# Kernel tuning notes

Measured on AMD Instinct MI355X. Metric: run time of the kernel, lower is better.

## Reference

```python
import jax, jax.numpy as jnp
import numpy as np

B, S, H, L = 64, 512, 768, 21


def setup_inputs() -> dict:
    key = jax.random.key(0)
    ks = jax.random.split(key, 8)
    hidden = jax.random.normal(ks[0], (B, S, H), dtype=jnp.float32)
    attention_mask = jnp.ones((B, S), dtype=jnp.int32)
    labels = jax.random.randint(ks[1], (B, S), 0, L, dtype=jnp.int64)
    W = jax.random.normal(ks[2], (H, L), dtype=jnp.float32) * 0.02
    b = jnp.zeros((L,), dtype=jnp.float32)
    start_transitions = jax.random.uniform(ks[3], (L,), minval=-0.1, maxval=0.1)
    end_transitions = jax.random.uniform(ks[4], (L,), minval=-0.1, maxval=0.1)
    transitions = jax.random.uniform(ks[5], (L, L), minval=-0.1, maxval=0.1)
    return {"hidden": hidden, "attention_mask": attention_mask, "labels": labels,
            "W": W, "b": b, "start_transitions": start_transitions,
            "end_transitions": end_transitions, "transitions": transitions}


def _crf_llh(emissions, tags, mask, start, end, trans):
    # torchcrf log-likelihood, batch_first. emissions [B,S,L], tags [B,S], mask [B,S] bool
    maskf = mask.astype(emissions.dtype)
    first_tags = tags[:, 0]
    num = start[first_tags] + jnp.take_along_axis(emissions[:, 0], first_tags[:, None], axis=1)[:, 0]
    trans_scores = trans[tags[:, :-1], tags[:, 1:]]                         # [B,S-1]
    emit_scores = jnp.take_along_axis(emissions, tags[:, :, None], axis=2)[:, :, 0]  # [B,S]
    num = num + jnp.sum((trans_scores + emit_scores[:, 1:]) * maskf[:, 1:], axis=1)
    seq_ends = jnp.sum(mask.astype(jnp.int32), axis=1) - 1
    last_tags = jnp.take_along_axis(tags, seq_ends[:, None], axis=1)[:, 0]
    num = num + end[last_tags]
    # denominator: forward algorithm as a scan over time
    def step(score, xs):
        emit_t, m_t = xs  # [B,L], [B]
        nxt = jax.nn.logsumexp(score[:, :, None] + trans[None] + emit_t[:, None, :], axis=1)
        return jnp.where(m_t[:, None], nxt, score), None
    score0 = start[None] + emissions[:, 0]
    xs = (jnp.transpose(emissions[:, 1:], (1, 0, 2)), mask[:, 1:].T)
    scoreT, _ = jax.lax.scan(step, score0, xs)
    denom = jax.nn.logsumexp(scoreT + end[None], axis=1)
    return num - denom


def _viterbi_one_hot(emissions, mask, start, end, trans):
    # Viterbi decode (max-plus scan) + backtrack, returns one-hot logits like _decoded_to_one_hot
    def fstep(score, xs):
        emit_t, m_t = xs
        cand = score[:, :, None] + trans[None]     # [B,L,L]
        idx = jnp.argmax(cand, axis=1)             # [B,L] best previous tag
        nxt = jnp.max(cand, axis=1) + emit_t
        return jnp.where(m_t[:, None], nxt, score), idx
    score0 = start[None] + emissions[:, 0]
    xs = (jnp.transpose(emissions[:, 1:], (1, 0, 2)), mask[:, 1:].T)
    scoreT, hist = jax.lax.scan(fstep, score0, xs)   # hist [S-1,B,L]
    best_last = jnp.argmax(scoreT + end[None], axis=1)  # [B]
    def bstep(carry, xs):
        h_t, m_t = xs
        prev = jnp.take_along_axis(h_t, carry[:, None], axis=1)[:, 0]
        return jnp.where(m_t, prev, carry), carry
    tag0, tags_rest = jax.lax.scan(bstep, best_last, (hist, mask[:, 1:].T), reverse=True)
    tags = jnp.concatenate([tag0[:, None], tags_rest.T], axis=1)  # [B,S]
    one_hot = jax.nn.one_hot(tags, emissions.shape[-1], dtype=emissions.dtype)
    return one_hot * mask[:, :, None].astype(emissions.dtype)


def reference(hidden, attention_mask, labels, W, b, start_transitions, end_transitions, transitions):
    mask = attention_mask.astype(bool)
    emissions = jnp.einsum('bsh,hl->bsl', hidden, W) + b  # classifier (dropout = identity in eval)
    logits = _viterbi_one_hot(emissions, mask, start_transitions, end_transitions, transitions)
    # loss path: replicate forward's tag/mask fixups
    tags = jnp.where(labels < 0, 0, labels).at[:, 0].set(0)
    valid = (mask & (labels >= 0)).at[:, 0].set(True)
    llh = _crf_llh(emissions, tags, valid, start_transitions, end_transitions, transitions)
    loss = -jnp.mean(llh)
    return loss, logits
```

## Files before the change

kernel.cpp:

```cpp
#include <hip/hip_runtime.h>
#include <math.h>

#define BB 64
#define SS 512
#define HH 768
#define LL 21
#define STR 513
#define INFF __builtin_huge_valf()

__device__ inline float rlf(float v, int i) {
    return __int_as_float(__builtin_amdgcn_readlane(__float_as_int(v), i));
}
__device__ inline float mx3(float a, float b, float c) { return fmaxf(fmaxf(a, b), c); }
__device__ inline float wmax64(float v) {
    #pragma unroll
    for (int off = 32; off; off >>= 1) v = fmaxf(v, __shfl_xor(v, off));
    return v;
}
__device__ inline float rlmax21(float a) {
    float r0 = mx3(rlf(a, 0), rlf(a, 1), rlf(a, 2));
    float r1 = mx3(rlf(a, 3), rlf(a, 4), rlf(a, 5));
    float r2 = mx3(rlf(a, 6), rlf(a, 7), rlf(a, 8));
    float r3 = mx3(rlf(a, 9), rlf(a, 10), rlf(a, 11));
    float r4 = mx3(rlf(a, 12), rlf(a, 13), rlf(a, 14));
    float r5 = mx3(rlf(a, 15), rlf(a, 16), rlf(a, 17));
    float r6 = mx3(rlf(a, 18), rlf(a, 19), rlf(a, 20));
    return mx3(mx3(r0, r1, r2), mx3(r3, r4, r5), r6);
}

__global__ __launch_bounds__(128) void k_emis(const float* __restrict__ hidden,
                                              const float* __restrict__ W,
                                              const float* __restrict__ bias,
                                              float* __restrict__ em0,
                                              float* __restrict__ em1) {
    __shared__ float Wl[384 * 24];
    int tid = threadIdx.x;
    int half = blockIdx.x & 1;
    int rb = blockIdx.x >> 1;
    int row = rb * 128 + tid;
    const float* hp = hidden + (size_t)row * HH + half * 384;
    const float4* Wh4 = reinterpret_cast<const float4*>(W + half * 384 * LL);

    for (int f = tid; f < 2016; f += 128) {
        float4 v = Wh4[f];
        int e0 = 4 * f;
        { int e = e0,     k = e / 21, l = e - 21 * k; Wl[k * 24 + l] = v.x; }
        { int e = e0 + 1, k = e / 21, l = e - 21 * k; Wl[k * 24 + l] = v.y; }
        { int e = e0 + 2, k = e / 21, l = e - 21 * k; Wl[k * 24 + l] = v.z; }
        { int e = e0 + 3, k = e / 21, l = e - 21 * k; Wl[k * 24 + l] = v.w; }
    }
    __syncthreads();

    float acc[LL];
    #pragma unroll
    for (int l = 0; l < LL; ++l) acc[l] = 0.f;

#define FMAK(HV, WB) do { \
    float hv_ = (HV); \
    float4 q0 = *reinterpret_cast<const float4*>(WB); \
    float4 q1 = *reinterpret_cast<const float4*>((WB) + 4); \
    float4 q2 = *reinterpret_cast<const float4*>((WB) + 8); \
    float4 q3 = *reinterpret_cast<const float4*>((WB) + 12); \
    float4 q4 = *reinterpret_cast<const float4*>((WB) + 16); \
    float q20 = (WB)[20]; \
    acc[0]  = fmaf(hv_, q0.x, acc[0]);  acc[1]  = fmaf(hv_, q0.y, acc[1]); \
    acc[2]  = fmaf(hv_, q0.z, acc[2]);  acc[3]  = fmaf(hv_, q0.w, acc[3]); \
    acc[4]  = fmaf(hv_, q1.x, acc[4]);  acc[5]  = fmaf(hv_, q1.y, acc[5]); \
    acc[6]  = fmaf(hv_, q1.z, acc[6]);  acc[7]  = fmaf(hv_, q1.w, acc[7]); \
    acc[8]  = fmaf(hv_, q2.x, acc[8]);  acc[9]  = fmaf(hv_, q2.y, acc[9]); \
    acc[10] = fmaf(hv_, q2.z, acc[10]); acc[11] = fmaf(hv_, q2.w, acc[11]); \
    acc[12] = fmaf(hv_, q3.x, acc[12]); acc[13] = fmaf(hv_, q3.y, acc[13]); \
    acc[14] = fmaf(hv_, q3.z, acc[14]); acc[15] = fmaf(hv_, q3.w, acc[15]); \
    acc[16] = fmaf(hv_, q4.x, acc[16]); acc[17] = fmaf(hv_, q4.y, acc[17]); \
    acc[18] = fmaf(hv_, q4.z, acc[18]); acc[19] = fmaf(hv_, q4.w, acc[19]); \
    acc[20] = fmaf(hv_, q20, acc[20]); } while (0)

    float4 ha = *reinterpret_cast<const float4*>(hp);
    for (int c = 0; c < 96; ++c) {
        float4 hn = ha;
        if (c + 1 < 96) hn = *reinterpret_cast<const float4*>(hp + (c + 1) * 4);
        const float* wb = Wl + (c * 4) * 24;
        FMAK(ha.x, wb);
        FMAK(ha.y, wb + 24);
        FMAK(ha.z, wb + 48);
        FMAK(ha.w, wb + 72);
        ha = hn;
    }
#undef FMAK

    float* emr = (half ? em1 : em0) + (size_t)row * LL;
    if (half) {
        #pragma unroll
        for (int l = 0; l < LL; ++l) emr[l] = acc[l];
    } else {
        #pragma unroll
        for (int l = 0; l < LL; ++l) emr[l] = acc[l] + bias[l];
    }
}

__global__ __launch_bounds__(64) void k_scan(const float* __restrict__ em0,
                                             const float* __restrict__ em1,
                                             const int* __restrict__ attn,
                                             const int* __restrict__ labels,
                                             const float* __restrict__ startT,
                                             const float* __restrict__ endT,
                                             const float* __restrict__ trans,
                                             float* __restrict__ num,
                                             float* __restrict__ denom,
                                             float* __restrict__ Sout) {
    __shared__ float eLT[LL * STR + 8];
    int lane = threadIdx.x;
    int bid = blockIdx.x;
    bool act = lane < LL;
    int jj = act ? lane : (LL - 1);

    if (bid < 128) {
        int b = bid & 63;
        const float* emb0 = em0 + (size_t)b * SS * LL;
        const float* emb1 = em1 + (size_t)b * SS * LL;
        const int* mrow = attn + b * SS;

        for (int f = lane; f < (SS * LL) / 4; f += 64) {
            float4 v0 = *reinterpret_cast<const float4*>(emb0 + 4 * f);
            float4 v1 = *reinterpret_cast<const float4*>(emb1 + 4 * f);
            float4 v = make_float4(v0.x + v1.x, v0.y + v1.y, v0.z + v1.z, v0.w + v1.w);
            unsigned e0 = 4u * (unsigned)f;
            { unsigned t = e0 / 21u,       j = e0 - 21u * t;       eLT[j * STR + t] = v.x; }
            { unsigned e = e0 + 1, t = e / 21u, j = e - 21u * t;   eLT[j * STR + t] = v.y; }
            { unsigned e = e0 + 2, t = e / 21u, j = e - 21u * t;   eLT[j * STR + t] = v.z; }
            { unsigned e = e0 + 3, t = e / 21u, j = e - 21u * t;   eLT[j * STR + t] = v.w; }
        }
        __syncthreads();

        int jbase = jj * STR;
        float A0, A1, A2, A3, B0, B1, B2, B3;

#define LDG(P, G) do { int t4_ = (G) * 4; \
    P##0 = eLT[jbase + t4_];     P##1 = eLT[jbase + t4_ + 1]; \
    P##2 = eLT[jbase + t4_ + 2]; P##3 = eLT[jbase + t4_ + 3]; } while (0)

        if (bid < 64) {
            float Tc[LL];
            #pragma unroll
            for (int i = 0; i < LL; ++i) Tc[i] = trans[i * LL + jj];
            float* Sgj = Sout + (size_t)b * (LL * SS) + jj * SS;

#define VCORE(EMIT, BIT) do { \
    float sv_[LL]; \
    _Pragma("unroll") for (int i_ = 0; i_ < LL; ++i_) sv_[i_] = rlf(a, i_); \
    __builtin_amdgcn_sched_barrier(0); \
    float cd_[LL]; \
    _Pragma("unroll") for (int i_ = 0; i_ < LL; ++i_) cd_[i_] = sv_[i_] + Tc[i_]; \
    float x0 = mx3(cd_[0], cd_[1], cd_[2]),   x1 = mx3(cd_[3], cd_[4], cd_[5]); \
    float x2 = mx3(cd_[6], cd_[7], cd_[8]),   x3 = mx3(cd_[9], cd_[10], cd_[11]); \
    float x4 = mx3(cd_[12], cd_[13], cd_[14]), x5 = mx3(cd_[15], cd_[16], cd_[17]); \
    float x6 = mx3(cd_[18], cd_[19], cd_[20]); \
    float best = mx3(mx3(x0, x1, x2), mx3(x3, x4, x5), x6); \
    bool mt_ = ((mm >> (BIT)) & 1ull) != 0ull; \
    float an_ = best + (EMIT); \
    a = (mt_ && act) ? an_ : a; \
} while (0)
#define VGROUPR(P, TB, BB0) do { \
    float o0_, o1_, o2_, o3_; \
    VCORE(P##0, (BB0));     o0_ = a; \
    VCORE(P##1, (BB0) + 1); o1_ = a; \
    VCORE(P##2, (BB0) + 2); o2_ = a; \
    VCORE(P##3, (BB0) + 3); o3_ = a; \
    if (act) *reinterpret_cast<float4*>(Sgj + (TB)) = make_float4(o0_, o1_, o2_, o3_); \
} while (0)

            LDG(A, 0); LDG(B, 1);
            int mk0 = mrow[lane];
            unsigned long long mm = __ballot(mk0 != 0);
            mk0 = mrow[64 + lane];
            float a = act ? (startT[lane] + A0) : -INFF;
            {
                float o0_ = a, o1_, o2_, o3_;
                VCORE(A1, 1); o1_ = a;
                VCORE(A2, 2); o2_ = a;
                VCORE(A3, 3); o3_ = a;
                if (act) *reinterpret_cast<float4*>(Sgj) = make_float4(o0_, o1_, o2_, o3_);
                LDG(A, 2);
                VGROUPR(B, 4, 4);
                LDG(B, 3);
            }
            for (int gg = 1; gg < 64; ++gg) {
                if ((gg & 7) == 0) {
                    mm = __ballot(mk0 != 0);
                    if (gg != 56) mk0 = mrow[((gg >> 3) + 1) * 64 + lane];
                }
                int bb = (gg & 7) * 8;
                VGROUPR(A, 8 * gg, bb);
                LDG(A, 2 * gg + 2);
                VGROUPR(B, 8 * gg + 4, bb + 4);
                LDG(B, 2 * gg + 3);
            }
#undef VCORE
#undef VGROUPR
        } else {
            float Ec[LL];
            #pragma unroll
            for (int i = 0; i < LL; ++i) Ec[i] = __expf(trans[i * LL + jj]);

#define LCORE(EMIT, BIT) do { \
    float x_ = __expf(a - M); \
    float sv_[LL]; \
    _Pragma("unroll") for (int i_ = 0; i_ < LL; ++i_) sv_[i_] = rlf(x_, i_); \
    __builtin_amdgcn_sched_barrier(0); \
    float g0_ = sv_[0] * Ec[0]; \
    _Pragma("unroll") for (int i_ = 1; i_ < 7; ++i_)  g0_ = fmaf(sv_[i_], Ec[i_], g0_); \
    float g1_ = sv_[7] * Ec[7]; \
    _Pragma("unroll") for (int i_ = 8; i_ < 14; ++i_) g1_ = fmaf(sv_[i_], Ec[i_], g1_); \
    float g2_ = sv_[14] * Ec[14]; \
    _Pragma("unroll") for (int i_ = 15; i_ < 21; ++i_) g2_ = fmaf(sv_[i_], Ec[i_], g2_); \
    float Ss_ = (g0_ + g1_) + g2_; \
    bool mt_ = ((mm >> (BIT)) & 1ull) != 0ull; \
    float an_ = M + __logf(Ss_) + (EMIT); \
    a = (mt_ && act) ? an_ : a; \
} while (0)

            LDG(A, 0); LDG(B, 1);
            int mk0 = mrow[lane];
            unsigned long long mm = __ballot(mk0 != 0);
            mk0 = mrow[64 + lane];
            float a = act ? (startT[lane] + A0) : -INFF;
            float M = rlmax21(a);
            {
                LCORE(A1, 1); LCORE(A2, 2); LCORE(A3, 3);
                LDG(A, 2);
                LCORE(B0, 4); LCORE(B1, 5); LCORE(B2, 6); LCORE(B3, 7);
                LDG(B, 3);
            }
            for (int gg = 1; gg < 64; ++gg) {
                if ((gg & 7) == 0) {
                    mm = __ballot(mk0 != 0);
                    if (gg != 56) mk0 = mrow[((gg >> 3) + 1) * 64 + lane];
                }
                M = rlmax21(a);
                int bb = (gg & 7) * 8;
                LCORE(A0, bb);     LCORE(A1, bb + 1); LCORE(A2, bb + 2); LCORE(A3, bb + 3);
                LDG(A, 2 * gg + 2);
                LCORE(B0, bb + 4); LCORE(B1, bb + 5); LCORE(B2, bb + 6); LCORE(B3, bb + 7);
                LDG(B, 2 * gg + 3);
            }
#undef LCORE
            float f = act ? (a + endT[lane]) : -INFF;
            float m = wmax64(f);
            float p = act ? __expf(f - m) : 0.f;
            #pragma unroll
            for (int off = 32; off; off >>= 1) p += __shfl_xor(p, off);
            if (lane == 0) denom[b] = m + __logf(p);
        }
#undef LDG
    } else {
        int b = bid - 128;
        const int* lrow = labels + b * SS;
        const int* arow = attn + b * SS;
        float psum = 0.f;
        int pcnt = 0;
        for (int s = 0; s < 8; ++s) {
            int t = s * 64 + lane;
            int lab = lrow[t];
            int mk = arow[t];
            int valid = (t == 0) ? 1 : ((mk != 0 && lab >= 0) ? 1 : 0);
            if (t >= 1 && valid) {
                int tag = (lab < 0) ? 0 : lab;
                int labp = lrow[t - 1];
                int tagp = (t == 1) ? 0 : ((labp < 0) ? 0 : labp);
                size_t ei = ((size_t)b * SS + t) * LL + tag;
                psum += trans[tagp * LL + tag] + em0[ei] + em1[ei];
            }
            pcnt += valid;
        }
        #pragma unroll
        for (int off = 32; off; off >>= 1) {
            psum += __shfl_xor(psum, off);
            pcnt += __shfl_xor(pcnt, off);
        }
        int ts = pcnt - 1;
        int labL = lrow[ts];
        int tagL = (ts == 0) ? 0 : ((labL < 0) ? 0 : labL);
        if (lane == 0) {
            size_t e0i = (size_t)b * SS * LL;
            num[b] = startT[0] + em0[e0i] + em1[e0i] + psum + endT[tagL];
        }
    }
}

__global__ __launch_bounds__(256) void k_back(const float* __restrict__ S,
                                              const int* __restrict__ attn,
                                              const float* __restrict__ endT,
                                              const float* __restrict__ trans,
                                              int* __restrict__ tagsOut) {
    __shared__ float Sl[LL][517];
    __shared__ unsigned char pred[SS * 24];
    __shared__ unsigned char mapL[64 * 32];
    __shared__ float Tl[441];
    int tid = threadIdx.x, b = blockIdx.x;
    const float* SB = S + (size_t)b * (LL * SS);
    for (int i = tid; i < 441; i += 256) Tl[i] = trans[i];
    for (int f = tid; f < (LL * SS) / 4; f += 256) {
        float4 v = *reinterpret_cast<const float4*>(SB + 4 * f);
        int j = f >> 7, t0 = (f & 127) * 4;
        Sl[j][t0] = v.x; Sl[j][t0 + 1] = v.y; Sl[j][t0 + 2] = v.z; Sl[j][t0 + 3] = v.w;
    }
    __syncthreads();

    for (int u = tid; u < 511 * LL; u += 256) {
        int t = 1 + u / LL;
        int j = u - (u / LL) * LL;
        unsigned int pj = (unsigned int)j;
        if (attn[b * SS + t] != 0) {
            float bv = Sl[0][t - 1] + Tl[j];
            unsigned int bi = 0;
            #pragma unroll
            for (int i = 1; i < LL; ++i) {
                float c = Sl[i][t - 1] + Tl[i * LL + j];
                bool g = c > bv;
                bv = g ? c : bv;
                bi = g ? (unsigned int)i : bi;
            }
            pj = bi;
        }
        pred[t * 24 + j] = (unsigned char)pj;
    }
    __syncthreads();

    if (tid < 64) {
        int lane = tid;
        float f = (lane < LL) ? (Sl[lane][SS - 1] + endT[lane]) : -INFF;
        float m = wmax64(f);
        unsigned long long msk = __ballot(f == m);
        int best_last = __ffsll(msk) - 1;

        int tlo = 8 * lane + 1;
        int thi = 8 * lane + 8; if (thi > 511) thi = 511;
        unsigned int BM[LL];
        #pragma unroll
        for (int s = 0; s < LL; ++s) BM[s] = s;
        for (int k = 0; k < 8; ++k) {
            int t = thi - k;
            if (t >= tlo) {
                #pragma unroll
                for (int s = 0; s < LL; ++s) BM[s] = pred[t * 24 + BM[s]];
            }
        }
        #pragma unroll
        for (int s = 0; s < LL; ++s) mapL[lane * 32 + s] = (unsigned char)BM[s];

        #pragma unroll
        for (int kk = 1; kk < 64; kk <<= 1) {
            int p = lane + kk;
            bool vld = p < 64;
            int pp = vld ? p : 0;
            unsigned int P[LL];
            #pragma unroll
            for (int s = 0; s < LL; ++s) {
                unsigned int v = mapL[pp * 32 + s];
                P[s] = vld ? v : (unsigned int)s;
            }
            unsigned int N[LL];
            #pragma unroll
            for (int s = 0; s < LL; ++s) N[s] = mapL[lane * 32 + P[s]];
            #pragma unroll
            for (int s = 0; s < LL; ++s) mapL[lane * 32 + s] = (unsigned char)N[s];
        }

        int st8 = mapL[lane * 32 + best_last];
        int nxt = __shfl(st8, lane + 1);
        int cur = (lane == 63) ? best_last : nxt;
        for (int k = 0; k < 8; ++k) {
            int t = thi - k;
            if (t >= tlo) {
                tagsOut[b * SS + t] = cur;
                cur = pred[t * 24 + cur];
            }
        }
        if (lane == 0) tagsOut[b * SS] = cur;
    }
}

__global__ __launch_bounds__(256) void k_out(const float* __restrict__ num,
                                             const float* __restrict__ denom,
                                             const int* __restrict__ tagsW,
                                             const int* __restrict__ attn,
                                             float* __restrict__ out) {
    int gid = blockIdx.x * 256 + threadIdx.x;
    if ((int)blockIdx.x == (int)gridDim.x - 1 && threadIdx.x < 64) {
        float llh = num[threadIdx.x] - denom[threadIdx.x];
        #pragma unroll
        for (int off = 32; off; off >>= 1) llh += __shfl_xor(llh, off);
        if (threadIdx.x == 0) out[0] = -llh / (float)BB;
    }
    if (gid < BB * SS * LL) {
        int bt = gid / LL, l = gid % LL;
        int tag = tagsW[bt];
        int mk  = attn[bt];
        out[1 + gid] = (mk && tag == l) ? 1.f : 0.f;
    }
}

extern "C" void kernel_launch(void* const* d_in, const int* in_sizes, int n_in,
                              void* d_out, int out_size, void* d_ws, size_t ws_size,
                              hipStream_t stream) {
    const float* hidden = (const float*)d_in[0];
    const int*   attn   = (const int*)d_in[1];
    const int*   labels = (const int*)d_in[2];
    const float* W      = (const float*)d_in[3];
    const float* bias   = (const float*)d_in[4];
    const float* startT = (const float*)d_in[5];
    const float* endT   = (const float*)d_in[6];
    const float* trans  = (const float*)d_in[7];
    float* out = (float*)d_out;

    float* wsf   = (float*)d_ws;
    float* em0   = wsf;
    float* em1   = em0 + (size_t)BB * SS * LL;
    float* num   = em1 + (size_t)BB * SS * LL;
    float* denom = num + 64;
    int*   tags  = (int*)(denom + 64);
    float* Sbuf  = out + 4;

    hipLaunchKernelGGL(k_emis, dim3(512), dim3(128), 0, stream, hidden, W, bias, em0, em1);
    hipLaunchKernelGGL(k_scan, dim3(192), dim3(64),  0, stream, em0, em1, attn, labels,
                       startT, endT, trans, num, denom, Sbuf);
    hipLaunchKernelGGL(k_back, dim3(64),  dim3(256), 0, stream, Sbuf, attn, endT, trans, tags);
    int oh_blocks = (BB * SS * LL + 255) / 256;
    hipLaunchKernelGGL(k_out,  dim3(oh_blocks + 1), dim3(256), 0, stream,
                       num, denom, tags, attn, out);
}
```

Baseline: 160.6 us.

## Drop LDS staging in CRF scan; stream emissions from global with deeper prefetch

The scan kernel no longer copies and transposes each batch's emissions into shared memory before starting the recurrence. Each wave now reads its per-tag emission values straight from the two global partial buffers, prefetching four groups of timesteps ahead instead of two. Waves are packed 12 per 768-thread block, so 16 blocks launch instead of 192 single-wave blocks. This removes the serial staging phase and barrier at the cost of strided global loads (about 21 floats apart) on the critical path and more live registers.

```diff
diff --git a/kernel.cpp b/kernel.cpp
--- a/kernel.cpp
+++ b/kernel.cpp
@@ -5,7 +5,6 @@
 #define SS 512
 #define HH 768
 #define LL 21
-#define STR 513
 #define INFF __builtin_huge_valf()
 
 __device__ inline float rlf(float v, int i) {
@@ -98,48 +97,39 @@
     }
 }
 
-__global__ __launch_bounds__(64) void k_scan(const float* __restrict__ em0,
-                                             const float* __restrict__ em1,
-                                             const int* __restrict__ attn,
-                                             const int* __restrict__ labels,
-                                             const float* __restrict__ startT,
-                                             const float* __restrict__ endT,
-                                             const float* __restrict__ trans,
-                                             float* __restrict__ num,
-                                             float* __restrict__ denom,
-                                             float* __restrict__ Sout) {
-    __shared__ float eLT[LL * STR + 8];
-    int lane = threadIdx.x;
-    int bid = blockIdx.x;
+__global__ __launch_bounds__(768) void k_scan(const float* __restrict__ em0,
+                                              const float* __restrict__ em1,
+                                              const int* __restrict__ attn,
+                                              const int* __restrict__ labels,
+                                              const float* __restrict__ startT,
+                                              const float* __restrict__ endT,
+                                              const float* __restrict__ trans,
+                                              float* __restrict__ num,
+                                              float* __restrict__ denom,
+                                              float* __restrict__ Sout) {
+    int gw = blockIdx.x * 12 + (threadIdx.x >> 6);
+    int lane = threadIdx.x & 63;
     bool act = lane < LL;
     int jj = act ? lane : (LL - 1);
 
-    if (bid < 128) {
-        int b = bid & 63;
-        const float* emb0 = em0 + (size_t)b * SS * LL;
-        const float* emb1 = em1 + (size_t)b * SS * LL;
+    if (gw < 128) {
+        int b = gw & 63;
+        const float* e0p = em0 + (size_t)b * SS * LL;
+        const float* e1p = em1 + (size_t)b * SS * LL;
         const int* mrow = attn + b * SS;
 
-        for (int f = lane; f < (SS * LL) / 4; f += 64) {
-            float4 v0 = *reinterpret_cast<const float4*>(emb0 + 4 * f);
-            float4 v1 = *reinterpret_cast<const float4*>(emb1 + 4 * f);
-            float4 v = make_float4(v0.x + v1.x, v0.y + v1.y, v0.z + v1.z, v0.w + v1.w);
-            unsigned e0 = 4u * (unsigned)f;
-            { unsigned t = e0 / 21u,       j = e0 - 21u * t;       eLT[j * STR + t] = v.x; }
-            { unsigned e = e0 + 1, t = e / 21u, j = e - 21u * t;   eLT[j * STR + t] = v.y; }
-            { unsigned e = e0 + 2, t = e / 21u, j = e - 21u * t;   eLT[j * STR + t] = v.z; }
-            { unsigned e = e0 + 3, t = e / 21u, j = e - 21u * t;   eLT[j * STR + t] = v.w; }
-        }
-        __syncthreads();
-
-        int jbase = jj * STR;
-        float A0, A1, A2, A3, B0, B1, B2, B3;
-
-#define LDG(P, G) do { int t4_ = (G) * 4; \
-    P##0 = eLT[jbase + t4_];     P##1 = eLT[jbase + t4_ + 1]; \
-    P##2 = eLT[jbase + t4_ + 2]; P##3 = eLT[jbase + t4_ + 3]; } while (0)
-
-        if (bid < 64) {
+        float Ae0, Ae1, Ae2, Ae3, Af0, Af1, Af2, Af3;
+        float Be0, Be1, Be2, Be3, Bf0, Bf1, Bf2, Bf3;
+        float Ce0, Ce1, Ce2, Ce3, Cf0, Cf1, Cf2, Cf3;
+        float De0, De1, De2, De3, Df0, Df1, Df2, Df3;
+
+#define LDG(P, G) do { size_t o_ = (size_t)(G) * 4 * LL + jj; \
+    P##e0 = e0p[o_];          P##f0 = e1p[o_]; \
+    P##e1 = e0p[o_ + LL];     P##f1 = e1p[o_ + LL]; \
+    P##e2 = e0p[o_ + 2 * LL]; P##f2 = e1p[o_ + 2 * LL]; \
+    P##e3 = e0p[o_ + 3 * LL]; P##f3 = e1p[o_ + 3 * LL]; } while (0)
+
+        if (gw < 64) {
             float Tc[LL];
             #pragma unroll
             for (int i = 0; i < LL; ++i) Tc[i] = trans[i * LL + jj];
@@ -160,40 +150,43 @@
     float an_ = best + (EMIT); \
     a = (mt_ && act) ? an_ : a; \
 } while (0)
-#define VGROUPR(P, TB, BB0) do { \
+#define VGROUPR(P, TB, BITB) do { \
     float o0_, o1_, o2_, o3_; \
-    VCORE(P##0, (BB0));     o0_ = a; \
-    VCORE(P##1, (BB0) + 1); o1_ = a; \
-    VCORE(P##2, (BB0) + 2); o2_ = a; \
-    VCORE(P##3, (BB0) + 3); o3_ = a; \
+    VCORE(P##e0 + P##f0, (BITB));     o0_ = a; \
+    VCORE(P##e1 + P##f1, (BITB) + 1); o1_ = a; \
+    VCORE(P##e2 + P##f2, (BITB) + 2); o2_ = a; \
+    VCORE(P##e3 + P##f3, (BITB) + 3); o3_ = a; \
     if (act) *reinterpret_cast<float4*>(Sgj + (TB)) = make_float4(o0_, o1_, o2_, o3_); \
 } while (0)
 
-            LDG(A, 0); LDG(B, 1);
-            int mk0 = mrow[lane];
-            unsigned long long mm = __ballot(mk0 != 0);
-            mk0 = mrow[64 + lane];
-            float a = act ? (startT[lane] + A0) : -INFF;
+            LDG(A, 0); LDG(B, 1); LDG(C, 2); LDG(D, 3);
+            int mkc = mrow[lane];
+            unsigned long long mm = __ballot(mkc != 0);
+            mkc = mrow[64 + lane];
+            float a = act ? (startT[lane] + (Ae0 + Af0)) : -INFF;
             {
                 float o0_ = a, o1_, o2_, o3_;
-                VCORE(A1, 1); o1_ = a;
-                VCORE(A2, 2); o2_ = a;
-                VCORE(A3, 3); o3_ = a;
+                VCORE(Ae1 + Af1, 1); o1_ = a;
+                VCORE(Ae2 + Af2, 2); o2_ = a;
+                VCORE(Ae3 + Af3, 3); o3_ = a;
                 if (act) *reinterpret_cast<float4*>(Sgj) = make_float4(o0_, o1_, o2_, o3_);
-                LDG(A, 2);
-                VGROUPR(B, 4, 4);
-                LDG(B, 3);
-            }
-            for (int gg = 1; gg < 64; ++gg) {
-                if ((gg & 7) == 0) {
-                    mm = __ballot(mk0 != 0);
-                    if (gg != 56) mk0 = mrow[((gg >> 3) + 1) * 64 + lane];
+                LDG(A, 4);
+                VGROUPR(B, 4, 4);   LDG(B, 5);
+                VGROUPR(C, 8, 8);   LDG(C, 6);
+                VGROUPR(D, 12, 12); LDG(D, 7);
+            }
+            for (int s = 1; s < 32; ++s) {
+                if ((s & 3) == 0) {
+                    mm = __ballot(mkc != 0);
+                    int blk = s >> 2;
+                    if (blk < 7) mkc = mrow[(blk + 1) * 64 + lane];
                 }
-                int bb = (gg & 7) * 8;
-                VGROUPR(A, 8 * gg, bb);
-                LDG(A, 2 * gg + 2);
-                VGROUPR(B, 8 * gg + 4, bb + 4);
-                LDG(B, 2 * gg + 3);
+                int g0 = 4 * s;
+                int bitb = (g0 & 15) * 4;
+                VGROUPR(A, g0 * 4,      bitb);      if (s < 31) LDG(A, g0 + 4);
+                VGROUPR(B, g0 * 4 + 4,  bitb + 4);  if (s < 31) LDG(B, g0 + 5);
+                VGROUPR(C, g0 * 4 + 8,  bitb + 8);  if (s < 31) LDG(C, g0 + 6);
+                VGROUPR(D, g0 * 4 + 12, bitb + 12); if (s < 31) LDG(D, g0 + 7);
             }
 #undef VCORE
 #undef VGROUPR
@@ -219,29 +212,48 @@
     a = (mt_ && act) ? an_ : a; \
 } while (0)
 
-            LDG(A, 0); LDG(B, 1);
-            int mk0 = mrow[lane];
-            unsigned long long mm = __ballot(mk0 != 0);
-            mk0 = mrow[64 + lane];
-            float a = act ? (startT[lane] + A0) : -INFF;
+            LDG(A, 0); LDG(B, 1); LDG(C, 2); LDG(D, 3);
+            int mkc = mrow[lane];
+            unsigned long long mm = __ballot(mkc != 0);
+            mkc = mrow[64 + lane];
+            float a = act ? (startT[lane] + (Ae0 + Af0)) : -INFF;
             float M = rlmax21(a);
             {
-                LCORE(A1, 1); LCORE(A2, 2); LCORE(A3, 3);
-                LDG(A, 2);
-                LCORE(B0, 4); LCORE(B1, 5); LCORE(B2, 6); LCORE(B3, 7);
-                LDG(B, 3);
-            }
-            for (int gg = 1; gg < 64; ++gg) {
-                if ((gg & 7) == 0) {
-                    mm = __ballot(mk0 != 0);
-                    if (gg != 56) mk0 = mrow[((gg >> 3) + 1) * 64 + lane];
+                LCORE(Ae1 + Af1, 1); LCORE(Ae2 + Af2, 2); LCORE(Ae3 + Af3, 3);
+                LDG(A, 4);
+                LCORE(Be0 + Bf0, 4); LCORE(Be1 + Bf1, 5);
+                LCORE(Be2 + Bf2, 6); LCORE(Be3 + Bf3, 7);
+                LDG(B, 5);
+                M = rlmax21(a);
+                LCORE(Ce0 + Cf0, 8);  LCORE(Ce1 + Cf1, 9);
+                LCORE(Ce2 + Cf2, 10); LCORE(Ce3 + Cf3, 11);
+                LDG(C, 6);
+                LCORE(De0 + Df0, 12); LCORE(De1 + Df1, 13);
+                LCORE(De2 + Df2, 14); LCORE(De3 + Df3, 15);
+                LDG(D, 7);
+            }
+            for (int s = 1; s < 32; ++s) {
+                if ((s & 3) == 0) {
+                    mm = __ballot(mkc != 0);
+                    int blk = s >> 2;
+                    if (blk < 7) mkc = mrow[(blk + 1) * 64 + lane];
                 }
+                int g0 = 4 * s;
+                int bitb = (g0 & 15) * 4;
                 M = rlmax21(a);
-                int bb = (gg & 7) * 8;
-                LCORE(A0, bb);     LCORE(A1, bb + 1); LCORE(A2, bb + 2); LCORE(A3, bb + 3);
-                LDG(A, 2 * gg + 2);
-                LCORE(B0, bb + 4); LCORE(B1, bb + 5); LCORE(B2, bb + 6); LCORE(B3, bb + 7);
-                LDG(B, 2 * gg + 3);
+                LCORE(Ae0 + Af0, bitb);     LCORE(Ae1 + Af1, bitb + 1);
+                LCORE(Ae2 + Af2, bitb + 2); LCORE(Ae3 + Af3, bitb + 3);
+                if (s < 31) LDG(A, g0 + 4);
+                LCORE(Be0 + Bf0, bitb + 4); LCORE(Be1 + Bf1, bitb + 5);
+                LCORE(Be2 + Bf2, bitb + 6); LCORE(Be3 + Bf3, bitb + 7);
+                if (s < 31) LDG(B, g0 + 5);
+                M = rlmax21(a);
+                LCORE(Ce0 + Cf0, bitb + 8);  LCORE(Ce1 + Cf1, bitb + 9);
+                LCORE(Ce2 + Cf2, bitb + 10); LCORE(Ce3 + Cf3, bitb + 11);
+                if (s < 31) LDG(C, g0 + 6);
+                LCORE(De0 + Df0, bitb + 12); LCORE(De1 + Df1, bitb + 13);
+                LCORE(De2 + Df2, bitb + 14); LCORE(De3 + Df3, bitb + 15);
+                if (s < 31) LDG(D, g0 + 7);
             }
 #undef LCORE
             float f = act ? (a + endT[lane]) : -INFF;
@@ -253,7 +265,7 @@
         }
 #undef LDG
     } else {
-        int b = bid - 128;
+        int b = gw - 128;
         const int* lrow = labels + b * SS;
         const int* arow = attn + b * SS;
         float psum = 0.f;
@@ -422,7 +434,7 @@
     float* Sbuf  = out + 4;
 
     hipLaunchKernelGGL(k_emis, dim3(512), dim3(128), 0, stream, hidden, W, bias, em0, em1);
-    hipLaunchKernelGGL(k_scan, dim3(192), dim3(64),  0, stream, em0, em1, attn, labels,
+    hipLaunchKernelGGL(k_scan, dim3(16),  dim3(768), 0, stream, em0, em1, attn, labels,
                        startT, endT, trans, num, denom, Sbuf);
     hipLaunchKernelGGL(k_back, dim3(64),  dim3(256), 0, stream, Sbuf, attn, endT, trans, tags);
     int oh_blocks = (BB * SS * LL + 255) / 256;
```

After: 279.2 us. 1.74x slower.

## Split emission GEMV into four H-quarters and widen backtrack blocks to 512

Applied to the files above, without the earlier changes.

The emission projection now splits the hidden dimension into four quarters instead of two, launching 1024 blocks, each with a smaller shared W tile. This raises the block count so the GPU's compute units are better filled. The scan kernel sums four partial buffers instead of two, which adds global reads and workspace. The backtrack kernel also goes from 256 to 512 threads per block to speed up the predecessor computation, at the cost of more registers per block.

```diff
diff --git a/kernel.cpp b/kernel.cpp
--- a/kernel.cpp
+++ b/kernel.cpp
@@ -32,17 +32,19 @@
                                               const float* __restrict__ W,
                                               const float* __restrict__ bias,
                                               float* __restrict__ em0,
-                                              float* __restrict__ em1) {
-    __shared__ float Wl[384 * 24];
+                                              float* __restrict__ em1,
+                                              float* __restrict__ em2,
+                                              float* __restrict__ em3) {
+    __shared__ float Wl[192 * 24];
     int tid = threadIdx.x;
-    int half = blockIdx.x & 1;
-    int rb = blockIdx.x >> 1;
-    int row = rb * 128 + tid;
-    const float* hp = hidden + (size_t)row * HH + half * 384;
-    const float4* Wh4 = reinterpret_cast<const float4*>(W + half * 384 * LL);
-
-    for (int f = tid; f < 2016; f += 128) {
-        float4 v = Wh4[f];
+    int q = blockIdx.x & 3;
+    int rg = blockIdx.x >> 2;
+    int row = rg * 128 + tid;
+    const float* hp = hidden + (size_t)row * HH + q * 192;
+    const float4* Wq4 = reinterpret_cast<const float4*>(W + q * 192 * LL);
+
+    for (int f = tid; f < 1008; f += 128) {
+        float4 v = Wq4[f];
         int e0 = 4 * f;
         { int e = e0,     k = e / 21, l = e - 21 * k; Wl[k * 24 + l] = v.x; }
         { int e = e0 + 1, k = e / 21, l = e - 21 * k; Wl[k * 24 + l] = v.y; }
@@ -76,9 +78,9 @@
     acc[20] = fmaf(hv_, q20, acc[20]); } while (0)
 
     float4 ha = *reinterpret_cast<const float4*>(hp);
-    for (int c = 0; c < 96; ++c) {
+    for (int c = 0; c < 48; ++c) {
         float4 hn = ha;
-        if (c + 1 < 96) hn = *reinterpret_cast<const float4*>(hp + (c + 1) * 4);
+        if (c + 1 < 48) hn = *reinterpret_cast<const float4*>(hp + (c + 1) * 4);
         const float* wb = Wl + (c * 4) * 24;
         FMAK(ha.x, wb);
         FMAK(ha.y, wb + 24);
@@ -88,18 +90,20 @@
     }
 #undef FMAK
 
-    float* emr = (half ? em1 : em0) + (size_t)row * LL;
-    if (half) {
+    float* emr = (q == 0 ? em0 : q == 1 ? em1 : q == 2 ? em2 : em3) + (size_t)row * LL;
+    if (q == 0) {
+        #pragma unroll
+        for (int l = 0; l < LL; ++l) emr[l] = acc[l] + bias[l];
+    } else {
         #pragma unroll
         for (int l = 0; l < LL; ++l) emr[l] = acc[l];
-    } else {
-        #pragma unroll
-        for (int l = 0; l < LL; ++l) emr[l] = acc[l] + bias[l];
     }
 }
 
 __global__ __launch_bounds__(64) void k_scan(const float* __restrict__ em0,
                                              const float* __restrict__ em1,
+                                             const float* __restrict__ em2,
+                                             const float* __restrict__ em3,
                                              const int* __restrict__ attn,
                                              const int* __restrict__ labels,
                                              const float* __restrict__ startT,
@@ -116,14 +120,22 @@
 
     if (bid < 128) {
         int b = bid & 63;
-        const float* emb0 = em0 + (size_t)b * SS * LL;
-        const float* emb1 = em1 + (size_t)b * SS * LL;
+        size_t boff = (size_t)b * SS * LL;
+        const float* emb0 = em0 + boff;
+        const float* emb1 = em1 + boff;
+        const float* emb2 = em2 + boff;
+        const float* emb3 = em3 + boff;
         const int* mrow = attn + b * SS;
 
         for (int f = lane; f < (SS * LL) / 4; f += 64) {
             float4 v0 = *reinterpret_cast<const float4*>(emb0 + 4 * f);
             float4 v1 = *reinterpret_cast<const float4*>(emb1 + 4 * f);
-            float4 v = make_float4(v0.x + v1.x, v0.y + v1.y, v0.z + v1.z, v0.w + v1.w);
+            float4 v2 = *reinterpret_cast<const float4*>(emb2 + 4 * f);
+            float4 v3 = *reinterpret_cast<const float4*>(emb3 + 4 * f);
+            float4 v = make_float4((v0.x + v1.x) + (v2.x + v3.x),
+                                   (v0.y + v1.y) + (v2.y + v3.y),
+                                   (v0.z + v1.z) + (v2.z + v3.z),
+                                   (v0.w + v1.w) + (v2.w + v3.w));
             unsigned e0 = 4u * (unsigned)f;
             { unsigned t = e0 / 21u,       j = e0 - 21u * t;       eLT[j * STR + t] = v.x; }
             { unsigned e = e0 + 1, t = e / 21u, j = e - 21u * t;   eLT[j * STR + t] = v.y; }
@@ -268,7 +280,7 @@
                 int labp = lrow[t - 1];
                 int tagp = (t == 1) ? 0 : ((labp < 0) ? 0 : labp);
                 size_t ei = ((size_t)b * SS + t) * LL + tag;
-                psum += trans[tagp * LL + tag] + em0[ei] + em1[ei];
+                psum += trans[tagp * LL + tag] + ((em0[ei] + em1[ei]) + (em2[ei] + em3[ei]));
             }
             pcnt += valid;
         }
@@ -282,12 +294,13 @@
         int tagL = (ts == 0) ? 0 : ((labL < 0) ? 0 : labL);
         if (lane == 0) {
             size_t e0i = (size_t)b * SS * LL;
-            num[b] = startT[0] + em0[e0i] + em1[e0i] + psum + endT[tagL];
-        }
-    }
-}
-
-__global__ __launch_bounds__(256) void k_back(const float* __restrict__ S,
+            num[b] = startT[0] + ((em0[e0i] + em1[e0i]) + (em2[e0i] + em3[e0i]))
+                   + psum + endT[tagL];
+        }
+    }
+}
+
+__global__ __launch_bounds__(512) void k_back(const float* __restrict__ S,
                                               const int* __restrict__ attn,
                                               const float* __restrict__ endT,
                                               const float* __restrict__ trans,
@@ -298,15 +311,15 @@
     __shared__ float Tl[441];
     int tid = threadIdx.x, b = blockIdx.x;
     const float* SB = S + (size_t)b * (LL * SS);
-    for (int i = tid; i < 441; i += 256) Tl[i] = trans[i];
-    for (int f = tid; f < (LL * SS) / 4; f += 256) {
+    for (int i = tid; i < 441; i += 512) Tl[i] = trans[i];
+    for (int f = tid; f < (LL * SS) / 4; f += 512) {
         float4 v = *reinterpret_cast<const float4*>(SB + 4 * f);
         int j = f >> 7, t0 = (f & 127) * 4;
         Sl[j][t0] = v.x; Sl[j][t0 + 1] = v.y; Sl[j][t0 + 2] = v.z; Sl[j][t0 + 3] = v.w;
     }
     __syncthreads();
 
-    for (int u = tid; u < 511 * LL; u += 256) {
+    for (int u = tid; u < 511 * LL; u += 512) {
         int t = 1 + u / LL;
         int j = u - (u / LL) * LL;
         unsigned int pj = (unsigned int)j;
@@ -414,17 +427,21 @@
     float* out = (float*)d_out;
 
     float* wsf   = (float*)d_ws;
+    size_t emsz  = (size_t)BB * SS * LL;
     float* em0   = wsf;
-    float* em1   = em0 + (size_t)BB * SS * LL;
-    float* num   = em1 + (size_t)BB * SS * LL;
+    float* em1   = em0 + emsz;
+    float* em2   = em1 + emsz;
+    float* em3   = em2 + emsz;
+    float* num   = em3 + emsz;
     float* denom = num + 64;
     int*   tags  = (int*)(denom + 64);
     float* Sbuf  = out + 4;
 
-    hipLaunchKernelGGL(k_emis, dim3(512), dim3(128), 0, stream, hidden, W, bias, em0, em1);
-    hipLaunchKernelGGL(k_scan, dim3(192), dim3(64),  0, stream, em0, em1, attn, labels,
-                       startT, endT, trans, num, denom, Sbuf);
-    hipLaunchKernelGGL(k_back, dim3(64),  dim3(256), 0, stream, Sbuf, attn, endT, trans, tags);
+    hipLaunchKernelGGL(k_emis, dim3(1024), dim3(128), 0, stream, hidden, W, bias,
+                       em0, em1, em2, em3);
+    hipLaunchKernelGGL(k_scan, dim3(192), dim3(64),  0, stream, em0, em1, em2, em3,
+                       attn, labels, startT, endT, trans, num, denom, Sbuf);
+    hipLaunchKernelGGL(k_back, dim3(64),  dim3(512), 0, stream, Sbuf, attn, endT, trans, tags);
     int oh_blocks = (BB * SS * LL + 255) / 256;
     hipLaunchKernelGGL(k_out,  dim3(oh_blocks + 1), dim3(256), 0, stream,
                        num, denom, tags, attn, out);
```

Result: faster. 149.0 us (-7.2%).
